# Optimization experiments

Hardware: AMD Instinct MI355X
Metric: run time of the kernel (lower is better)

The kernel has to match this reference:

```python
import jax, jax.numpy as jnp
import numpy as np

N = 100000   # nodes
E = 1600000  # edges (avg degree 16)
D = 128      # feature dim (in_size == out_size)
L = 3        # n_layers

def setup_inputs() -> dict:
    key = jax.random.key(0)
    k0, k1, k2, k3, k4 = jax.random.split(key, 5)
    x = jax.random.normal(k0, (N, D), dtype=jnp.float32)
    src = jax.random.randint(k1, (E,), 0, N)
    dst = jax.random.randint(k2, (E,), 0, N)
    # positive edge weights (DGL EdgeWeightNorm requires nonnegative)
    edge_weight = jax.random.uniform(k3, (E,), dtype=jnp.float32) + 0.1
    W = jax.random.normal(k4, (L, D, D), dtype=jnp.float32) / np.float32(np.sqrt(D))
    b = jnp.zeros((L, D), dtype=jnp.float32)
    return {"x": x, "edge_weight": edge_weight, "W": W, "b": b, "src": src, "dst": dst}

def reference(x, edge_weight, W, b, src, dst):
    n = x.shape[0]
    # EdgeWeightNorm(norm='both'): w_ij / sqrt(deg_out_w(src_i) * deg_in_w(dst_j))
    deg_src = jax.ops.segment_sum(edge_weight, src, num_segments=n)  # weighted out-degree
    deg_dst = jax.ops.segment_sum(edge_weight, dst, num_segments=n)  # weighted in-degree
    nw = edge_weight * jax.lax.rsqrt(deg_src[src] * deg_dst[dst])    # [E]
    h = x
    for i in range(W.shape[0]):
        # GraphConv(norm='none'): transform, weighted-sum aggregate, bias, ELU
        h = h @ W[i]                                   # [N, D]
        msg = h[src] * nw[:, None]                     # [E, D] gather + scale
        h = jax.ops.segment_sum(msg, dst, num_segments=n) + b[i]
        h = jax.nn.elu(h)
    return h
```

## Files before the change

### kernel.cpp

```cpp
#include <hip/hip_runtime.h>
#include <hip/hip_bf16.h>


#define D128 128
#define PBLK 256
#define BUCKET_SHIFT 8
#define DCAP 7168

typedef __attribute__((ext_vector_type(8))) short s8v;
typedef __attribute__((ext_vector_type(16))) float f16v;

__device__ __forceinline__ float elu1(float x) {
    return x > 0.f ? x : (expf(x) - 1.f);
}

__device__ __forceinline__ unsigned short bf16_rne(float v) {
    unsigned u = __float_as_uint(v);
    return (unsigned short)((u + 0x7fffu + ((u >> 16) & 1u)) >> 16);
}


__global__ __launch_bounds__(256) void part_hist2(
    const int* __restrict__ src, const int* __restrict__ dst,
    int* __restrict__ histT2, int E, int nb, int chunk, int hlen) {
    extern __shared__ int sh[];
    for (int i = threadIdx.x; i < 2 * nb; i += 256) sh[i] = 0;
    __syncthreads();
    int b = blockIdx.x;
    int beg = b * chunk, end = min(E, beg + chunk);
    for (int e = beg + threadIdx.x; e < end; e += 256) {
        atomicAdd(&sh[dst[e] >> BUCKET_SHIFT], 1);
        atomicAdd(&sh[nb + (src[e] >> BUCKET_SHIFT)], 1);
    }
    __syncthreads();
    for (int i = threadIdx.x; i < nb; i += 256)
        histT2[i * PBLK + b] = sh[i];
    for (int i = threadIdx.x; i < nb; i += 256)
        histT2[hlen + i * PBLK + b] = sh[nb + i];
}

__global__ __launch_bounds__(256) void scan_block(
    const int* __restrict__ in, int* __restrict__ out,
    int* __restrict__ blockSums, int n) {
    __shared__ int tmp[256];
    int gid = blockIdx.x * 256 + threadIdx.x;
    int v = (gid < n) ? in[gid] : 0;
    tmp[threadIdx.x] = v;
    __syncthreads();
    for (int off = 1; off < 256; off <<= 1) {
        int t = (threadIdx.x >= off) ? tmp[threadIdx.x - off] : 0;
        __syncthreads();
        tmp[threadIdx.x] += t;
        __syncthreads();
    }
    if (gid < n) out[gid] = tmp[threadIdx.x] - v;
    if (threadIdx.x == 255) blockSums[blockIdx.x] = tmp[255];
}

__global__ __launch_bounds__(1024) void scan_sums(int* __restrict__ bsums, int nb) {
    __shared__ int tmp[1024];
    int v = (threadIdx.x < nb) ? bsums[threadIdx.x] : 0;
    tmp[threadIdx.x] = v;
    __syncthreads();
    for (int off = 1; off < 1024; off <<= 1) {
        int t = (threadIdx.x >= off) ? tmp[threadIdx.x - off] : 0;
        __syncthreads();
        tmp[threadIdx.x] += t;
        __syncthreads();
    }
    if (threadIdx.x < nb) bsums[threadIdx.x] = tmp[threadIdx.x] - v;
}

__global__ __launch_bounds__(256) void part_scatter2(
    const int* __restrict__ src, const int* __restrict__ dst,
    const float* __restrict__ w, const int* __restrict__ offsT2,
    const int* __restrict__ bsums,
    int2* __restrict__ pkw, int2* __restrict__ skw,
    int E, int nb, int chunk, int hlen) {
    extern __shared__ int cur[];
    int b = blockIdx.x;
    for (int i = threadIdx.x; i < nb; i += 256)
        cur[i] = offsT2[i * PBLK + b] + bsums[i];
    for (int i = threadIdx.x; i < nb; i += 256)
        cur[nb + i] = offsT2[hlen + i * PBLK + b] + bsums[nb + i] - E;
    __syncthreads();
    int beg = b * chunk, end = min(E, beg + chunk);
    for (int e = beg + threadIdx.x; e < end; e += 256) {
        int d = dst[e];
        int s = src[e];
        int wv = __float_as_int(w[e]);
        int kd = d >> BUCKET_SHIFT;
        int pos = atomicAdd(&cur[kd], 1);
        pkw[pos] = make_int2((int)((unsigned)s | ((unsigned)(d & 255) << 24)), wv);
        int ks = s >> BUCKET_SHIFT;
        int posS = atomicAdd(&cur[nb + ks], 1);
        skw[posS] = make_int2(s & 255, wv);
    }
}

__global__ __launch_bounds__(256) void bucket_sumS(
    const int2* __restrict__ skw, const int* __restrict__ offsT2,
    const int* __restrict__ bsums,
    float* __restrict__ deg_src, int E, int nb, int N, int hlen) {
    __shared__ float wsum[256];
    int k = blockIdx.x;
    int base = offsT2[hlen + k * PBLK] + bsums[nb + k] - E;
    int end = (k + 1 < nb) ? (offsT2[hlen + (k + 1) * PBLK] + bsums[nb + k + 1] - E) : E;
    int t = threadIdx.x;
    wsum[t] = 0.f;
    __syncthreads();
    for (int i = base + t; i < end; i += 256) {
        int2 v = skw[i];
        atomicAdd(&wsum[v.x], __int_as_float(v.y));
    }
    __syncthreads();
    int node = (k << BUCKET_SHIFT) + t;
    if (node < N) deg_src[node] = wsum[t];
}

__global__ __launch_bounds__(256) void bucket_build(
    const int2* __restrict__ pkw, const int* __restrict__ offsT,
    const int* __restrict__ bsums, const float* __restrict__ deg_src,
    int* __restrict__ row_start, int2* __restrict__ edata,
    int E, int nb, int N) {
    __shared__ int cnt[256];
    __shared__ float wsum[256];
    __shared__ int loc[256];
    __shared__ int cur2[256];
    extern __shared__ int2 stage[];

    int k = blockIdx.x;
    int base = offsT[k * PBLK] + bsums[k];
    int end = (k + 1 < nb) ? (offsT[(k + 1) * PBLK] + bsums[k + 1]) : E;
    int m = end - base;
    int t = threadIdx.x;
    cnt[t] = 0;
    wsum[t] = 0.f;
    __syncthreads();
    bool staged = (m <= DCAP);
    for (int i = t; i < m; i += 256) {
        int2 kw = pkw[base + i];
        if (staged) stage[i] = kw;
        int dl = (unsigned)kw.x >> 24;
        atomicAdd(&cnt[dl], 1);
        atomicAdd(&wsum[dl], __int_as_float(kw.y));
    }
    __syncthreads();
    int v = cnt[t];
    loc[t] = v;
    __syncthreads();
    for (int off = 1; off < 256; off <<= 1) {
        int tv = (t >= off) ? loc[t - off] : 0;
        __syncthreads();
        loc[t] += tv;
        __syncthreads();
    }
    int excl = loc[t] - v;
    loc[t] = excl;
    cur2[t] = 0;
    int node = (k << BUCKET_SHIFT) + t;
    if (node < N) row_start[node] = base + excl;
    if (k == 0 && t == 0) row_start[N] = E;
    __syncthreads();
    for (int i = t; i < m; i += 256) {
        int2 kw = staged ? stage[i] : pkw[base + i];
        int dl = (unsigned)kw.x >> 24;
        int s = kw.x & 0xFFFFFF;
        int pos = base + loc[dl] + atomicAdd(&cur2[dl], 1);
        float nw = __int_as_float(kw.y) * rsqrtf(deg_src[s] * wsum[dl]);
        edata[pos] = make_int2(s, __float_as_int(nw));
    }
}


__global__ __launch_bounds__(256) void prep_w(
    const float* __restrict__ W, unsigned short* __restrict__ Wh,
    unsigned short* __restrict__ Wl, int total) {
    int i = blockIdx.x * 256 + threadIdx.x;
    if (i >= total) return;
    int l = i >> 14;
    int rem = i & 16383;
    int k = rem >> 7, nn = rem & 127;
    float v = W[i];
    unsigned short h = bf16_rne(v);
    float fh = __uint_as_float((unsigned)h << 16);
    unsigned short lo = bf16_rne(v - fh);
    size_t oi = ((((size_t)l * 16 + (k >> 3)) * 128 + nn) << 3) + (k & 7);
    Wh[oi] = h;
    Wl[oi] = lo;
}

__global__ __launch_bounds__(256) void gemm_mfma(
    const float* __restrict__ A, const unsigned short* __restrict__ Wh,
    const unsigned short* __restrict__ Wl, unsigned short* __restrict__ Hb,
    int n) {
    __shared__ s8v lds_hi[16][32];
    __shared__ s8v lds_lo[16][32];
    const int t = threadIdx.x;
    const int r0 = blockIdx.x * 32;
    const int l = t & 63;
    const int wv = t >> 6;
    const int n0 = wv * 32;
    const int lr = l & 31, lh = l >> 5;

    s8v bh[8], bl[8];
#pragma unroll
    for (int k0 = 0; k0 < 8; ++k0) {
        int kc = k0 * 2 + lh;
        size_t gi = ((size_t)kc * 128 + n0 + lr) << 3;
        bh[k0] = *(const s8v*)(Wh + gi);
        bl[k0] = *(const s8v*)(Wl + gi);
    }

    {
        int row = t >> 3;
        int kc0 = t & 7;
        int r = r0 + row;
#pragma unroll
        for (int hhalf = 0; hhalf < 2; ++hhalf) {
            int kc = kc0 + 8 * hhalf;
            float4 v0 = make_float4(0.f, 0.f, 0.f, 0.f), v1 = v0;
            if (r < n) {
                const float4* ap = (const float4*)(A + (size_t)r * D128 + kc * 8);
                v0 = ap[0];
                v1 = ap[1];
            }
            s8v sh, sl;
#pragma unroll
            for (int e = 0; e < 8; ++e) {
                float v = (e < 4) ? ((const float*)&v0)[e] : ((const float*)&v1)[e - 4];
                unsigned short h = bf16_rne(v);
                float fh = __uint_as_float((unsigned)h << 16);
                sh[e] = (short)h;
                sl[e] = (short)bf16_rne(v - fh);
            }
            lds_hi[kc][row ^ (kc & 7)] = sh;
            lds_lo[kc][row ^ (kc & 7)] = sl;
        }
    }
    __syncthreads();

    f16v acc = {0.f, 0.f, 0.f, 0.f, 0.f, 0.f, 0.f, 0.f,
                0.f, 0.f, 0.f, 0.f, 0.f, 0.f, 0.f, 0.f};
#pragma unroll
    for (int k0 = 0; k0 < 8; ++k0) {
        int kc = k0 * 2 + lh;
        s8v ah = lds_hi[kc][lr ^ (kc & 7)];
        s8v al = lds_lo[kc][lr ^ (kc & 7)];
        acc = __builtin_amdgcn_mfma_f32_32x32x16_bf16(ah, bh[k0], acc, 0, 0, 0);
        acc = __builtin_amdgcn_mfma_f32_32x32x16_bf16(ah, bl[k0], acc, 0, 0, 0);
        acc = __builtin_amdgcn_mfma_f32_32x32x16_bf16(al, bh[k0], acc, 0, 0, 0);
    }

#pragma unroll
    for (int rg = 0; rg < 16; ++rg) {
        int grow = r0 + (rg & 3) + 8 * (rg >> 2) + 4 * lh;
        if (grow < n) Hb[(size_t)grow * D128 + n0 + lr] = bf16_rne(acc[rg]);
    }
}


__global__ __launch_bounds__(256) void aggregate_bf16(
    const unsigned short* __restrict__ hb, const int* __restrict__ rs,
    const int2* __restrict__ edata,
    const float* __restrict__ bias, float* __restrict__ out, int n) {
    int wave = threadIdx.x >> 6;
    int lane = threadIdx.x & 63;
    int node = blockIdx.x * 4 + wave;
    if (node >= n) return;
    int beg = rs[node], end = rs[node + 1];
    int half = lane >> 5, c = lane & 31;
    float4 a0 = make_float4(0.f, 0.f, 0.f, 0.f);
    float4 a1 = a0, a2 = a0, a3 = a0;
    int i = beg + half;
    for (; i + 6 < end; i += 8) {
        int2 e0 = edata[i];
        int2 e1 = edata[i + 2];
        int2 e2 = edata[i + 4];
        int2 e3 = edata[i + 6];
        uint2 p0 = ((const uint2*)(hb + (size_t)e0.x * D128))[c];
        uint2 p1 = ((const uint2*)(hb + (size_t)e1.x * D128))[c];
        uint2 p2 = ((const uint2*)(hb + (size_t)e2.x * D128))[c];
        uint2 p3 = ((const uint2*)(hb + (size_t)e3.x * D128))[c];
        float w0 = __int_as_float(e0.y), w1 = __int_as_float(e1.y);
        float w2 = __int_as_float(e2.y), w3 = __int_as_float(e3.y);
        a0.x = fmaf(__uint_as_float(p0.x << 16), w0, a0.x);
        a0.y = fmaf(__uint_as_float(p0.x & 0xffff0000u), w0, a0.y);
        a0.z = fmaf(__uint_as_float(p0.y << 16), w0, a0.z);
        a0.w = fmaf(__uint_as_float(p0.y & 0xffff0000u), w0, a0.w);
        a1.x = fmaf(__uint_as_float(p1.x << 16), w1, a1.x);
        a1.y = fmaf(__uint_as_float(p1.x & 0xffff0000u), w1, a1.y);
        a1.z = fmaf(__uint_as_float(p1.y << 16), w1, a1.z);
        a1.w = fmaf(__uint_as_float(p1.y & 0xffff0000u), w1, a1.w);
        a2.x = fmaf(__uint_as_float(p2.x << 16), w2, a2.x);
        a2.y = fmaf(__uint_as_float(p2.x & 0xffff0000u), w2, a2.y);
        a2.z = fmaf(__uint_as_float(p2.y << 16), w2, a2.z);
        a2.w = fmaf(__uint_as_float(p2.y & 0xffff0000u), w2, a2.w);
        a3.x = fmaf(__uint_as_float(p3.x << 16), w3, a3.x);
        a3.y = fmaf(__uint_as_float(p3.x & 0xffff0000u), w3, a3.y);
        a3.z = fmaf(__uint_as_float(p3.y << 16), w3, a3.z);
        a3.w = fmaf(__uint_as_float(p3.y & 0xffff0000u), w3, a3.w);
    }
    for (; i < end; i += 2) {
        int2 e0 = edata[i];
        uint2 p0 = ((const uint2*)(hb + (size_t)e0.x * D128))[c];
        float w0 = __int_as_float(e0.y);
        a0.x = fmaf(__uint_as_float(p0.x << 16), w0, a0.x);
        a0.y = fmaf(__uint_as_float(p0.x & 0xffff0000u), w0, a0.y);
        a0.z = fmaf(__uint_as_float(p0.y << 16), w0, a0.z);
        a0.w = fmaf(__uint_as_float(p0.y & 0xffff0000u), w0, a0.w);
    }
    a0.x += a1.x + a2.x + a3.x;
    a0.y += a1.y + a2.y + a3.y;
    a0.z += a1.z + a2.z + a3.z;
    a0.w += a1.w + a2.w + a3.w;
    a0.x += __shfl_xor(a0.x, 32);
    a0.y += __shfl_xor(a0.y, 32);
    a0.z += __shfl_xor(a0.z, 32);
    a0.w += __shfl_xor(a0.w, 32);
    if (half == 0) {
        float4 bb = ((const float4*)bias)[c];
        float4 o;
        o.x = elu1(a0.x + bb.x);
        o.y = elu1(a0.y + bb.y);
        o.z = elu1(a0.z + bb.z);
        o.w = elu1(a0.w + bb.w);
        ((float4*)(out + (size_t)node * D128))[c] = o;
    }
}

extern "C" void kernel_launch(void* const* d_in, const int* in_sizes, int n_in,
                              void* d_out, int out_size, void* d_ws, size_t ws_size,
                              hipStream_t stream) {
    const float* x   = (const float*)d_in[0];
    const float* ew  = (const float*)d_in[1];
    const float* W   = (const float*)d_in[2];
    const float* b   = (const float*)d_in[3];
    const int*   src = (const int*)d_in[4];
    const int*   dst = (const int*)d_in[5];
    float* out = (float*)d_out;

    const int N = in_sizes[0] / D128;
    const int E = in_sizes[1];
    const int L = in_sizes[2] / (D128 * D128);
    const int nb = (N + 255) >> BUCKET_SHIFT;
    const int hlen = nb * PBLK;

    char* ws = (char*)d_ws;
    size_t off = 0;
    auto take = [&](size_t bytes) {
        void* p = ws + off;
        off = (off + bytes + 255) & ~(size_t)255;
        return p;
    };
    float* deg_src = (float*)take((size_t)N * 4);
    int*   histT2  = (int*)take((size_t)2 * hlen * 4);
    int*   offsT2  = (int*)take((size_t)2 * hlen * 4);
    int*   bsums   = (int*)take(1024 * 4);
    int*   rstart  = (int*)take((size_t)(N + 1) * 4);
    int2*  edata   = (int2*)take((size_t)E * 8);
    unsigned short* Hb = (unsigned short*)take((size_t)N * D128 * 2);
    unsigned short* Whg = (unsigned short*)take((size_t)L * D128 * D128 * 2);
    unsigned short* Wlg = (unsigned short*)take((size_t)L * D128 * D128 * 2);
    int2* pkw = (int2*)Hb;
    int2* skw = ((int2*)Hb) + E;

    const int chunk = (E + PBLK - 1) / PBLK;
    const int sb2 = (2 * hlen + 255) / 256;
    const size_t part_lds = (size_t)2 * nb * 4;
    const size_t dcap_lds = (size_t)DCAP * 8;

    const int wtotal = L * D128 * D128;
    prep_w<<<(wtotal + 255) / 256, 256, 0, stream>>>(W, Whg, Wlg, wtotal);

    part_hist2<<<PBLK, 256, part_lds, stream>>>(src, dst, histT2, E, nb, chunk, hlen);
    scan_block<<<sb2, 256, 0, stream>>>(histT2, offsT2, bsums, 2 * hlen);
    scan_sums<<<1, 1024, 0, stream>>>(bsums, sb2);
    part_scatter2<<<PBLK, 256, part_lds, stream>>>(src, dst, ew, offsT2, bsums,
                                                   pkw, skw, E, nb, chunk, hlen);
    bucket_sumS<<<nb, 256, 0, stream>>>(skw, offsT2, bsums, deg_src, E, nb, N, hlen);
    bucket_build<<<nb, 256, dcap_lds, stream>>>(pkw, offsT2, bsums, deg_src,
                                                rstart, edata, E, nb, N);

    const int gemm_grid = (N + 31) / 32;
    const int agg_grid = (N + 3) / 4;

    gemm_mfma<<<gemm_grid, 256, 0, stream>>>(x, Whg, Wlg, Hb, N);
    aggregate_bf16<<<agg_grid, 256, 0, stream>>>(Hb, rstart, edata, b, out, N);
    for (int l = 1; l < L; ++l) {
        gemm_mfma<<<gemm_grid, 256, 0, stream>>>(
            out, Whg + (size_t)l * D128 * D128, Wlg + (size_t)l * D128 * D128, Hb, N);
        aggregate_bf16<<<agg_grid, 256, 0, stream>>>(Hb, rstart, edata,
                                                     b + (size_t)l * D128, out, N);
    }
}
```

Baseline: 364.7 us.

## Store intermediate layer activations in bf16 and add bf16-input GEMM kernel

Intermediate aggregate outputs are now written as bf16 into a separate buffer instead of fp32. A new GEMM kernel reads those bf16 activations directly, processes 64 rows per block, and drops the low-part A correction MFMA. This halves activation write and read traffic between layers and removes the split work on A. In exchange it loses precision on intermediate activations, and the layer loop is hardcoded to three layers. The scan is also made in-place, which frees the separate offsets buffer.

```diff
diff --git a/kernel.cpp b/kernel.cpp
--- a/kernel.cpp
+++ b/kernel.cpp
@@ -40,11 +40,10 @@
 }
 
 __global__ __launch_bounds__(256) void scan_block(
-    const int* __restrict__ in, int* __restrict__ out,
-    int* __restrict__ blockSums, int n) {
+    int* __restrict__ data, int* __restrict__ blockSums, int n) {
     __shared__ int tmp[256];
     int gid = blockIdx.x * 256 + threadIdx.x;
-    int v = (gid < n) ? in[gid] : 0;
+    int v = (gid < n) ? data[gid] : 0;
     tmp[threadIdx.x] = v;
     __syncthreads();
     for (int off = 1; off < 256; off <<= 1) {
@@ -53,7 +52,7 @@
         tmp[threadIdx.x] += t;
         __syncthreads();
     }
-    if (gid < n) out[gid] = tmp[threadIdx.x] - v;
+    if (gid < n) data[gid] = tmp[threadIdx.x] - v;
     if (threadIdx.x == 255) blockSums[blockIdx.x] = tmp[255];
 }
 
@@ -190,7 +189,7 @@
     Wl[oi] = lo;
 }
 
-__global__ __launch_bounds__(256) void gemm_mfma(
+__global__ __launch_bounds__(256) void gemm_mfma_f32(
     const float* __restrict__ A, const unsigned short* __restrict__ Wh,
     const unsigned short* __restrict__ Wl, unsigned short* __restrict__ Hb,
     int n) {
@@ -259,11 +258,68 @@
     }
 }
 
+__global__ __launch_bounds__(256) void gemm_mfma_bf16(
+    const unsigned short* __restrict__ A, const unsigned short* __restrict__ Wh,
+    const unsigned short* __restrict__ Wl, unsigned short* __restrict__ Hb,
+    int n) {
+    __shared__ s8v lds_a[16][64];
+    const int t = threadIdx.x;
+    const int r0 = blockIdx.x * 64;
+    const int l = t & 63;
+    const int wv = t >> 6;
+    const int n0 = wv * 32;
+    const int lr = l & 31, lh = l >> 5;
+
+    s8v bh[8], bl[8];
+#pragma unroll
+    for (int k0 = 0; k0 < 8; ++k0) {
+        int kc = k0 * 2 + lh;
+        size_t gi = ((size_t)kc * 128 + n0 + lr) << 3;
+        bh[k0] = *(const s8v*)(Wh + gi);
+        bl[k0] = *(const s8v*)(Wl + gi);
+    }
+
+#pragma unroll
+    for (int g4 = 0; g4 < 4; ++g4) {
+        int g = t * 4 + g4;
+        int row = g >> 4, kc = g & 15;
+        int r = r0 + row;
+        s8v v = {0, 0, 0, 0, 0, 0, 0, 0};
+        if (r < n) v = *(const s8v*)(A + (size_t)r * D128 + kc * 8);
+        lds_a[kc][row ^ (kc & 7)] = v;
+    }
+    __syncthreads();
+
+    f16v acc0 = {0.f, 0.f, 0.f, 0.f, 0.f, 0.f, 0.f, 0.f,
+                 0.f, 0.f, 0.f, 0.f, 0.f, 0.f, 0.f, 0.f};
+    f16v acc1 = acc0;
+#pragma unroll
+    for (int k0 = 0; k0 < 8; ++k0) {
+        int kc = k0 * 2 + lh;
+        s8v a0 = lds_a[kc][lr ^ (kc & 7)];
+        s8v a1 = lds_a[kc][(32 + lr) ^ (kc & 7)];
+        acc0 = __builtin_amdgcn_mfma_f32_32x32x16_bf16(a0, bh[k0], acc0, 0, 0, 0);
+        acc0 = __builtin_amdgcn_mfma_f32_32x32x16_bf16(a0, bl[k0], acc0, 0, 0, 0);
+        acc1 = __builtin_amdgcn_mfma_f32_32x32x16_bf16(a1, bh[k0], acc1, 0, 0, 0);
+        acc1 = __builtin_amdgcn_mfma_f32_32x32x16_bf16(a1, bl[k0], acc1, 0, 0, 0);
+    }
+
+#pragma unroll
+    for (int rg = 0; rg < 16; ++rg) {
+        int rr = (rg & 3) + 8 * (rg >> 2) + 4 * lh;
+        int grow0 = r0 + rr;
+        int grow1 = r0 + 32 + rr;
+        if (grow0 < n) Hb[(size_t)grow0 * D128 + n0 + lr] = bf16_rne(acc0[rg]);
+        if (grow1 < n) Hb[(size_t)grow1 * D128 + n0 + lr] = bf16_rne(acc1[rg]);
+    }
+}
+
 
 __global__ __launch_bounds__(256) void aggregate_bf16(
     const unsigned short* __restrict__ hb, const int* __restrict__ rs,
-    const int2* __restrict__ edata,
-    const float* __restrict__ bias, float* __restrict__ out, int n) {
+    const int2* __restrict__ edata, const float* __restrict__ bias,
+    unsigned short* __restrict__ outb, float* __restrict__ outf,
+    int obf, int n) {
     int wave = threadIdx.x >> 6;
     int lane = threadIdx.x & 63;
     int node = blockIdx.x * 4 + wave;
@@ -325,7 +381,14 @@
         o.y = elu1(a0.y + bb.y);
         o.z = elu1(a0.z + bb.z);
         o.w = elu1(a0.w + bb.w);
-        ((float4*)(out + (size_t)node * D128))[c] = o;
+        if (obf) {
+            uint2 p;
+            p.x = (unsigned)bf16_rne(o.x) | ((unsigned)bf16_rne(o.y) << 16);
+            p.y = (unsigned)bf16_rne(o.z) | ((unsigned)bf16_rne(o.w) << 16);
+            ((uint2*)(outb + (size_t)node * D128))[c] = p;
+        } else {
+            ((float4*)(outf + (size_t)node * D128))[c] = o;
+        }
     }
 }
 
@@ -355,15 +418,15 @@
     };
     float* deg_src = (float*)take((size_t)N * 4);
     int*   histT2  = (int*)take((size_t)2 * hlen * 4);
-    int*   offsT2  = (int*)take((size_t)2 * hlen * 4);
     int*   bsums   = (int*)take(1024 * 4);
     int*   rstart  = (int*)take((size_t)(N + 1) * 4);
     int2*  edata   = (int2*)take((size_t)E * 8);
     unsigned short* Hb = (unsigned short*)take((size_t)N * D128 * 2);
+    unsigned short* Ab = (unsigned short*)take((size_t)N * D128 * 2);
     unsigned short* Whg = (unsigned short*)take((size_t)L * D128 * D128 * 2);
     unsigned short* Wlg = (unsigned short*)take((size_t)L * D128 * D128 * 2);
-    int2* pkw = (int2*)Hb;
-    int2* skw = ((int2*)Hb) + E;
+    int2* pkw = (int2*)Ab;
+    int2* skw = ((int2*)Ab) + E;
 
     const int chunk = (E + PBLK - 1) / PBLK;
     const int sb2 = (2 * hlen + 255) / 256;
@@ -374,23 +437,27 @@
     prep_w<<<(wtotal + 255) / 256, 256, 0, stream>>>(W, Whg, Wlg, wtotal);
 
     part_hist2<<<PBLK, 256, part_lds, stream>>>(src, dst, histT2, E, nb, chunk, hlen);
-    scan_block<<<sb2, 256, 0, stream>>>(histT2, offsT2, bsums, 2 * hlen);
+    scan_block<<<sb2, 256, 0, stream>>>(histT2, bsums, 2 * hlen);
     scan_sums<<<1, 1024, 0, stream>>>(bsums, sb2);
-    part_scatter2<<<PBLK, 256, part_lds, stream>>>(src, dst, ew, offsT2, bsums,
+    part_scatter2<<<PBLK, 256, part_lds, stream>>>(src, dst, ew, histT2, bsums,
                                                    pkw, skw, E, nb, chunk, hlen);
-    bucket_sumS<<<nb, 256, 0, stream>>>(skw, offsT2, bsums, deg_src, E, nb, N, hlen);
-    bucket_build<<<nb, 256, dcap_lds, stream>>>(pkw, offsT2, bsums, deg_src,
+    bucket_sumS<<<nb, 256, 0, stream>>>(skw, histT2, bsums, deg_src, E, nb, N, hlen);
+    bucket_build<<<nb, 256, dcap_lds, stream>>>(pkw, histT2, bsums, deg_src,
                                                 rstart, edata, E, nb, N);
 
-    const int gemm_grid = (N + 31) / 32;
+    const int g32 = (N + 31) / 32;
+    const int g64 = (N + 63) / 64;
     const int agg_grid = (N + 3) / 4;
 
-    gemm_mfma<<<gemm_grid, 256, 0, stream>>>(x, Whg, Wlg, Hb, N);
-    aggregate_bf16<<<agg_grid, 256, 0, stream>>>(Hb, rstart, edata, b, out, N);
-    for (int l = 1; l < L; ++l) {
-        gemm_mfma<<<gemm_grid, 256, 0, stream>>>(
-            out, Whg + (size_t)l * D128 * D128, Wlg + (size_t)l * D128 * D128, Hb, N);
-        aggregate_bf16<<<agg_grid, 256, 0, stream>>>(Hb, rstart, edata,
-                                                     b + (size_t)l * D128, out, N);
-    }
-}
+    gemm_mfma_f32<<<g32, 256, 0, stream>>>(x, Whg, Wlg, Hb, N);
+    aggregate_bf16<<<agg_grid, 256, 0, stream>>>(Hb, rstart, edata, b,
+                                                 Ab, nullptr, 1, N);
+    gemm_mfma_bf16<<<g64, 256, 0, stream>>>(Ab, Whg + D128 * D128,
+                                            Wlg + D128 * D128, Hb, N);
+    aggregate_bf16<<<agg_grid, 256, 0, stream>>>(Hb, rstart, edata, b + D128,
+                                                 Ab, nullptr, 1, N);
+    gemm_mfma_bf16<<<g64, 256, 0, stream>>>(Ab, Whg + 2 * D128 * D128,
+                                            Wlg + 2 * D128 * D128, Hb, N);
+    aggregate_bf16<<<agg_grid, 256, 0, stream>>>(Hb, rstart, edata, b + 2 * D128,
+                                                 nullptr, out, 0, N);
+}
```

Result: no change. 360.8 us (-1.1%).
